# Kernel tuning notes

Measured on AMD Instinct MI355X. Metric: run time of the kernel, lower is better.

## Reference

```python
import jax, jax.numpy as jnp
import numpy as np

GMO_SIGMA = 1.0
EPS_GMO = 1e-16
EPS_BARY = 1e-16
EPS_DIV = 1e-12
CHUNK = 512  # points per search chunk to bound [B, CHUNK, F] intermediates


def _tri_sqdist(p, a, b, c):
    """Exact squared point-to-triangle distance (Ericson).
    p: [B,Pc,1,3], a/b/c: [B,1,F,3] -> [B,Pc,F]"""
    ab = b - a
    ac = c - a
    ap = p - a
    d1 = (ab * ap).sum(-1)
    d2 = (ac * ap).sum(-1)
    bp = p - b
    d3 = (ab * bp).sum(-1)
    d4 = (ac * bp).sum(-1)
    cp_ = p - c
    d5 = (ab * cp_).sum(-1)
    d6 = (ac * cp_).sum(-1)
    va = d3 * d6 - d5 * d4
    vb = d5 * d2 - d1 * d6
    vc = d1 * d4 - d3 * d2
    # candidate closest points per region
    t_ab = d1 / jnp.maximum(d1 - d3, EPS_DIV)
    t_ac = d2 / jnp.maximum(d2 - d6, EPS_DIV)
    t_bc = (d4 - d3) / jnp.maximum((d4 - d3) + (d5 - d6), EPS_DIV)
    den = jnp.maximum(va + vb + vc, EPS_DIV)
    v = (vb / den)[..., None]
    w = (vc / den)[..., None]
    cp = a + v * ab + w * ac  # face interior (default)
    m_bc = (va <= 0) & ((d4 - d3) >= 0) & ((d5 - d6) >= 0)
    m_ac = (vb <= 0) & (d2 >= 0) & (d6 <= 0)
    m_ab = (vc <= 0) & (d1 >= 0) & (d3 <= 0)
    m_a = (d1 <= 0) & (d2 <= 0)
    m_b = (d3 >= 0) & (d4 <= d3)
    m_c = (d6 >= 0) & (d5 <= d6)
    cp = jnp.where(m_bc[..., None], b + t_bc[..., None] * (c - b), cp)
    cp = jnp.where(m_ac[..., None], a + t_ac[..., None] * ac, cp)
    cp = jnp.where(m_ab[..., None], a + t_ab[..., None] * ab, cp)
    cp = jnp.where(m_c[..., None], c, cp)
    cp = jnp.where(m_b[..., None], b, cp)
    cp = jnp.where(m_a[..., None], a, cp)
    return ((p - cp) ** 2).sum(-1)


def _nearest_face_idx(points, tri):
    """points: [B,P,3], tri: [B,F,3,3] -> int32 [B,P] index of nearest face."""
    B, P, _ = points.shape
    a = tri[:, None, :, 0, :]
    b = tri[:, None, :, 1, :]
    c = tri[:, None, :, 2, :]
    nC = P // CHUNK
    pts = points.reshape(B, nC, CHUNK, 3).transpose(1, 0, 2, 3)  # [nC,B,Pc,3]

    def chunk_fn(p):  # p: [B,Pc,3]
        d = _tri_sqdist(p[:, :, None, :], a, b, c)  # [B,Pc,F]
        return jnp.argmin(d, axis=-1)

    idx = jax.lax.map(chunk_fn, pts)  # [nC,B,Pc]
    return idx.transpose(1, 0, 2).reshape(B, P)


def _barycentric(a, b, c, q):
    v1 = b - a
    v2 = c - a
    n = jnp.cross(v1, v2)
    n_dot_n = (n * n).sum(-1)
    n_dot_n = jnp.where(n_dot_n < EPS_BARY, 1.0, n_dot_n)
    w = q - a
    gamma = (jnp.cross(v1, w) * n).sum(-1) / n_dot_n
    beta = (jnp.cross(w, v2) * n).sum(-1) / n_dot_n
    alpha = 1.0 - beta - gamma
    return jnp.stack((alpha, beta, gamma), axis=-1)


def _gmo(sqr_input, sigma):
    sqr_sigma = sigma ** 2
    return jnp.sqrt(sqr_sigma * (sqr_input / (sqr_sigma + sqr_input)) + EPS_GMO)


def setup_inputs() -> dict:
    key = jax.random.key(0)
    k1, k2, k3 = jax.random.split(key, 3)
    points = jax.random.normal(k1, (2, 2048, 3), dtype=jnp.float32)
    mesh_vertices = jax.random.normal(k2, (2, 2562, 3), dtype=jnp.float32)
    mesh_faces = jax.random.randint(k3, (5120, 3), 0, 2562, dtype=jnp.int32)
    return {"points": points, "mesh_vertices": mesh_vertices, "mesh_faces": mesh_faces}


def reference(points, mesh_vertices, mesh_faces):
    B, P, _ = points.shape
    tri = mesh_vertices[:, mesh_faces]  # [B,F,3,3] face vertices
    face_idx = _nearest_face_idx(points, tri)  # [B,P]
    closest_tri = jnp.take_along_axis(tri, face_idx[:, :, None, None], axis=1)  # [B,P,3,3]
    a = closest_tri[:, :, 0, :]
    b = closest_tri[:, :, 1, :]
    c = closest_tri[:, :, 2, :]
    bco = _barycentric(a, b, c, points)  # [B,P,3]
    closest_points = (a * bco[:, :, 0:1] + b * bco[:, :, 1:2] + c * bco[:, :, 2:3])
    square_distances = ((closest_points - points) ** 2).sum(-1)
    robust = _gmo(square_distances, GMO_SIGMA)
    return robust.mean(-1).mean()
```

## Files before the change

### kernel.cpp

```cpp
#include <hip/hip_runtime.h>
#include <math.h>

#define EPS_GMO  1e-16f
#define EPS_BARY 1e-16f
#define EPS_DIV  1e-12f
#define TPB  512
#define RTPB 256
#define GPTS 4
#define FSTRIDE 12
#define QCAP 2048

__global__ void gather_fdat_kernel(const float* __restrict__ verts,
                                   const int* __restrict__ faces,
                                   float* __restrict__ fdat,
                                   int B, int F, int V)
{
    int i = blockIdx.x * blockDim.x + threadIdx.x;
    if (i >= B * F) return;
    int b = i / F;
    int f = i - b * F;
    int i0 = faces[f * 3 + 0], i1 = faces[f * 3 + 1], i2 = faces[f * 3 + 2];
    const float* pa = verts + ((size_t)b * V + i0) * 3;
    const float* pb = verts + ((size_t)b * V + i1) * 3;
    const float* pc = verts + ((size_t)b * V + i2) * 3;
    float ax = pa[0], ay = pa[1], az = pa[2];
    float abx = pb[0] - ax, aby = pb[1] - ay, abz = pb[2] - az;
    float acx = pc[0] - ax, acy = pc[1] - ay, acz = pc[2] - az;
    float saa = abx * abx + aby * aby + abz * abz;
    float sab = abx * acx + aby * acy + abz * acz;
    float scc = acx * acx + acy * acy + acz * acz;
    float* o = fdat + (size_t)i * FSTRIDE;
    o[0] = ax;  o[1] = ay;  o[2] = az;
    o[3] = abx; o[4] = aby; o[5] = abz;
    o[6] = acx; o[7] = acy; o[8] = acz;
    o[9] = saa; o[10] = sab; o[11] = scc;
}

__device__ float tri_sqdist_exact(float px, float py, float pz,
                                  float ax, float ay, float az,
                                  float bx, float by, float bz,
                                  float cx, float cy, float cz)
{
#pragma clang fp contract(off)
    float abx = bx - ax, aby = by - ay, abz = bz - az;
    float acx = cx - ax, acy = cy - ay, acz = cz - az;
    float apx = px - ax, apy = py - ay, apz = pz - az;
    float d1 = abx * apx + aby * apy + abz * apz;
    float d2 = acx * apx + acy * apy + acz * apz;
    float bpx = px - bx, bpy = py - by, bpz = pz - bz;
    float d3 = abx * bpx + aby * bpy + abz * bpz;
    float d4 = acx * bpx + acy * bpy + acz * bpz;
    float cpx_ = px - cx, cpy_ = py - cy, cpz_ = pz - cz;
    float d5 = abx * cpx_ + aby * cpy_ + abz * cpz_;
    float d6 = acx * cpx_ + acy * cpy_ + acz * cpz_;
    float va = d3 * d6 - d5 * d4;
    float vb = d5 * d2 - d1 * d6;
    float vc = d1 * d4 - d3 * d2;
    float t_ab = d1 / fmaxf(d1 - d3, EPS_DIV);
    float t_ac = d2 / fmaxf(d2 - d6, EPS_DIV);
    float t_bc = (d4 - d3) / fmaxf((d4 - d3) + (d5 - d6), EPS_DIV);
    float den = fmaxf(va + vb + vc, EPS_DIV);
    float v = vb / den;
    float w = vc / den;
    float qx = ax + v * abx + w * acx;
    float qy = ay + v * aby + w * acy;
    float qz = az + v * abz + w * acz;
    bool m_bc = (va <= 0.0f) && (d4 - d3 >= 0.0f) && (d5 - d6 >= 0.0f);
    bool m_ac = (vb <= 0.0f) && (d2 >= 0.0f) && (d6 <= 0.0f);
    bool m_ab = (vc <= 0.0f) && (d1 >= 0.0f) && (d3 <= 0.0f);
    bool m_a  = (d1 <= 0.0f) && (d2 <= 0.0f);
    bool m_b  = (d3 >= 0.0f) && (d4 <= d3);
    bool m_c  = (d6 >= 0.0f) && (d5 <= d6);
    if (m_bc) { qx = bx + t_bc * (cx - bx); qy = by + t_bc * (cy - by); qz = bz + t_bc * (cz - bz); }
    if (m_ac) { qx = ax + t_ac * acx;       qy = ay + t_ac * acy;       qz = az + t_ac * acz; }
    if (m_ab) { qx = ax + t_ab * abx;       qy = ay + t_ab * aby;       qz = az + t_ab * abz; }
    if (m_c)  { qx = cx; qy = cy; qz = cz; }
    if (m_b)  { qx = bx; qy = by; qz = bz; }
    if (m_a)  { qx = ax; qy = ay; qz = az; }
    float dx = px - qx, dy = py - qy, dz = pz - qz;
    return dx * dx + dy * dy + dz * dz;
}

__device__ __forceinline__ int dcode(float d)
{
    unsigned raw = __float_as_uint(d) >> 21;
    int c = (int)raw - 380;
    return c < 0 ? 0 : (c > 255 ? 255 : c);
}

__global__ __launch_bounds__(TPB) void p2s_main_kernel(
    const float* __restrict__ points,
    const float* __restrict__ verts,
    const int* __restrict__ faces,
    const float* __restrict__ fdat,
    float* __restrict__ robust_out,
    int P, int V, int F, int npts)
{
    extern __shared__ unsigned dstore32[];
    __shared__ float sd[TPB];
    __shared__ int   si[TPB];
    __shared__ float sT[GPTS];
    __shared__ int   sFace[GPTS];
    __shared__ unsigned squeue[QCAP];
    __shared__ unsigned scnt;

    const int tid = threadIdx.x;
    const int gp0 = blockIdx.x * GPTS;
    const int b   = gp0 / P;

    if (tid == 0) scnt = 0;

    float px[GPTS], py[GPTS], pz[GPTS];
#pragma unroll
    for (int g = 0; g < GPTS; ++g) {
        int gp = gp0 + g; if (gp >= npts) gp = npts - 1;
        const float* pp = points + (size_t)gp * 3;
        px[g] = pp[0]; py[g] = pp[1]; pz[g] = pp[2];
    }

    const float* fb = fdat + (size_t)b * F * FSTRIDE;

    float best[GPTS];
#pragma unroll
    for (int g = 0; g < GPTS; ++g) best[g] = INFINITY;

    for (int f = tid; f < F; f += TPB) {
        const float* fd = fb + (size_t)f * FSTRIDE;
        float4 q0 = *(const float4*)(fd + 0);
        float4 q1 = *(const float4*)(fd + 4);
        float4 q2 = *(const float4*)(fd + 8);
        float ax = q0.x, ay = q0.y, az = q0.z;
        float abx = q0.w, aby = q1.x, abz = q1.y;
        float acx = q1.z, acy = q1.w, acz = q2.x;
        float saa = q2.y, sab = q2.z, scc = q2.w;
        float cbb = saa - 2.0f * sab + scc;
        float det = saa * scc - sab * sab;
        float rsaa = __builtin_amdgcn_rcpf(fmaxf(saa, 1e-30f));
        float rscc = __builtin_amdgcn_rcpf(fmaxf(scc, 1e-30f));
        float rcbb = __builtin_amdgcn_rcpf(fmaxf(cbb, 1e-30f));
        float rdet = __builtin_amdgcn_rcpf(fmaxf(det, 1e-30f));
        float k1 = saa - sab;
        unsigned wcode = 0;
#pragma unroll
        for (int g = 0; g < GPTS; ++g) {
            float apx = px[g] - ax, apy = py[g] - ay, apz = pz[g] - az;
            float sap = apx * apx + apy * apy + apz * apz;
            float d1 = apx * abx + apy * aby + apz * abz;
            float d2 = apx * acx + apy * acy + apz * acz;
            float t0 = __builtin_amdgcn_fmed3f(d1 * rsaa, 0.0f, 1.0f);
            float h0 = d1 + d1;
            float dab = sap - t0 * (h0 - t0 * saa);
            float t1 = __builtin_amdgcn_fmed3f(d2 * rscc, 0.0f, 1.0f);
            float dac = sap - t1 * ((d2 + d2) - t1 * scc);
            float e1 = (d2 - d1) + k1;
            float t2 = __builtin_amdgcn_fmed3f(e1 * rcbb, 0.0f, 1.0f);
            float bpp = (sap - h0) + saa;
            float dbc = bpp - t2 * ((e1 + e1) - t2 * cbb);
            float dmin = fminf(fminf(dab, dac), dbc);
            float vnum = scc * d1 - sab * d2;
            float wnum = saa * d2 - sab * d1;
            bool inside = (vnum >= 0.0f) & (wnum >= 0.0f) & ((vnum + wnum) <= det);
            float idist = sap - (vnum * d1 + wnum * d2) * rdet;
            float d = fmaxf(inside ? fminf(idist, dmin) : dmin, 0.0f);
            wcode |= (unsigned)dcode(d) << (8 * g);
            best[g] = fminf(best[g], d);
        }
        dstore32[f] = wcode;
    }

#pragma unroll
    for (int g = 0; g < GPTS; ++g) {
        sd[tid] = best[g];
        __syncthreads();
        for (int s = TPB / 2; s > 0; s >>= 1) {
            if (tid < s) sd[tid] = fminf(sd[tid], sd[tid + s]);
            __syncthreads();
        }
        if (tid == 0) sT[g] = sd[0] + (1e-4f + 1e-2f * sd[0]);
        __syncthreads();
    }

    int codeT[GPTS];
#pragma unroll
    for (int g = 0; g < GPTS; ++g) codeT[g] = dcode(sT[g]);

    for (int f = tid; f < F; f += TPB) {
        unsigned w = dstore32[f];
#pragma unroll
        for (int g = 0; g < GPTS; ++g) {
            if ((int)((w >> (8 * g)) & 0xffu) <= codeT[g]) {
                unsigned idx = atomicAdd(&scnt, 1u);
                if (idx < QCAP) squeue[idx] = ((unsigned)g << 13) | (unsigned)f;
            }
        }
    }
    __syncthreads();
    unsigned total = scnt;

    float bestE[GPTS]; int bestI[GPTS];
#pragma unroll
    for (int g = 0; g < GPTS; ++g) { bestE[g] = INFINITY; bestI[g] = 0x7fffffff; }

    if (total <= QCAP) {
        for (unsigned q = tid; q < total; q += TPB) {
            unsigned e = squeue[q];
            int g = (int)(e >> 13);
            int f = (int)(e & 0x1fffu);
            int i0 = faces[f * 3 + 0], i1 = faces[f * 3 + 1], i2 = faces[f * 3 + 2];
            const float* pa = verts + ((size_t)b * V + i0) * 3;
            const float* pbv = verts + ((size_t)b * V + i1) * 3;
            const float* pc = verts + ((size_t)b * V + i2) * 3;
            float de = tri_sqdist_exact(px[g], py[g], pz[g],
                                        pa[0], pa[1], pa[2],
                                        pbv[0], pbv[1], pbv[2],
                                        pc[0], pc[1], pc[2]);
            if (de < bestE[g] || (de == bestE[g] && f < bestI[g])) {
                bestE[g] = de; bestI[g] = f;
            }
        }
    } else {
        for (int f = tid; f < F; f += TPB) {
            unsigned w = dstore32[f];
            bool cg[GPTS]; bool any = false;
#pragma unroll
            for (int g = 0; g < GPTS; ++g) {
                cg[g] = (int)((w >> (8 * g)) & 0xffu) <= codeT[g];
                any = any || cg[g];
            }
            if (any) {
                int i0 = faces[f * 3 + 0], i1 = faces[f * 3 + 1], i2 = faces[f * 3 + 2];
                const float* pa = verts + ((size_t)b * V + i0) * 3;
                const float* pbv = verts + ((size_t)b * V + i1) * 3;
                const float* pc = verts + ((size_t)b * V + i2) * 3;
                float ax = pa[0], ay = pa[1], az = pa[2];
                float bx = pbv[0], by = pbv[1], bz = pbv[2];
                float cx = pc[0], cy = pc[1], cz = pc[2];
#pragma unroll
                for (int g = 0; g < GPTS; ++g) {
                    if (cg[g]) {
                        float de = tri_sqdist_exact(px[g], py[g], pz[g],
                                                    ax, ay, az, bx, by, bz, cx, cy, cz);
                        if (de < bestE[g]) { bestE[g] = de; bestI[g] = f; }
                    }
                }
            }
        }
    }

#pragma unroll
    for (int g = 0; g < GPTS; ++g) {
        sd[tid] = bestE[g]; si[tid] = bestI[g];
        __syncthreads();
        for (int s = TPB / 2; s > 0; s >>= 1) {
            if (tid < s) {
                float dv = sd[tid + s]; int iv = si[tid + s];
                if (dv < sd[tid] || (dv == sd[tid] && iv < si[tid])) { sd[tid] = dv; si[tid] = iv; }
            }
            __syncthreads();
        }
        if (tid == 0) sFace[g] = si[0];
        __syncthreads();
    }

    if (tid < GPTS) {
#pragma clang fp contract(off)
        int g = tid;
        int gp = gp0 + g;
        if (gp < npts) {
            int f = sFace[g];
            int i0 = faces[f * 3 + 0], i1 = faces[f * 3 + 1], i2 = faces[f * 3 + 2];
            const float* pa = verts + ((size_t)b * V + i0) * 3;
            const float* pbv = verts + ((size_t)b * V + i1) * 3;
            const float* pc = verts + ((size_t)b * V + i2) * 3;
            float ax = pa[0], ay = pa[1], az = pa[2];
            float bx = pbv[0], by = pbv[1], bz = pbv[2];
            float cx = pc[0], cy = pc[1], cz = pc[2];
            float Px = px[g], Py = py[g], Pz = pz[g];
            float v1x = bx - ax, v1y = by - ay, v1z = bz - az;
            float v2x = cx - ax, v2y = cy - ay, v2z = cz - az;
            float nx = v1y * v2z - v1z * v2y;
            float ny = v1z * v2x - v1x * v2z;
            float nz = v1x * v2y - v1y * v2x;
            float nn = nx * nx + ny * ny + nz * nz;
            if (nn < EPS_BARY) nn = 1.0f;
            float wx = Px - ax, wy = Py - ay, wz = Pz - az;
            float c1x = v1y * wz - v1z * wy;
            float c1y = v1z * wx - v1x * wz;
            float c1z = v1x * wy - v1y * wx;
            float gamma = (c1x * nx + c1y * ny + c1z * nz) / nn;
            float c2x = wy * v2z - wz * v2y;
            float c2y = wz * v2x - wx * v2z;
            float c2z = wx * v2y - wy * v2x;
            float beta = (c2x * nx + c2y * ny + c2z * nz) / nn;
            float alpha = 1.0f - beta - gamma;
            float cpx = ax * alpha + bx * beta + cx * gamma;
            float cpy = ay * alpha + by * beta + cy * gamma;
            float cpz = az * alpha + bz * beta + cz * gamma;
            float dx = cpx - Px, dy = cpy - Py, dz = cpz - Pz;
            float sdist = dx * dx + dy * dy + dz * dz;
            float r = sqrtf(sdist / (1.0f + sdist) + EPS_GMO);
            robust_out[gp] = r;
        }
    }
}

__global__ __launch_bounds__(RTPB) void reduce_mean_kernel(
    const float* __restrict__ vals, float* __restrict__ out, int N, float inv)
{
    __shared__ float s[RTPB];
    int tid = threadIdx.x;
    float acc = 0.0f;
    for (int i = tid; i < N; i += RTPB) acc += vals[i];
    s[tid] = acc;
    __syncthreads();
    for (int st = RTPB / 2; st > 0; st >>= 1) {
        if (tid < st) s[tid] += s[tid + st];
        __syncthreads();
    }
    if (tid == 0) out[0] = s[0] * inv;
}

extern "C" void kernel_launch(void* const* d_in, const int* in_sizes, int n_in,
                              void* d_out, int out_size, void* d_ws, size_t ws_size,
                              hipStream_t stream)
{
    const float* points = (const float*)d_in[0];
    const float* verts  = (const float*)d_in[1];
    const int*   faces  = (const int*)d_in[2];
    float* out = (float*)d_out;

    const int B = 2;
    const int P = in_sizes[0] / (B * 3);
    const int V = in_sizes[1] / (B * 3);
    const int F = in_sizes[2] / 3;
    const int npts = B * P;

    float* fdat   = (float*)d_ws;
    float* robust = fdat + (size_t)B * F * FSTRIDE;

    int nBF = B * F;
    gather_fdat_kernel<<<(nBF + RTPB - 1) / RTPB, RTPB, 0, stream>>>(verts, faces, fdat, B, F, V);

    int nBlocks = (npts + GPTS - 1) / GPTS;
    size_t dynLds = (size_t)F * sizeof(unsigned);
    p2s_main_kernel<<<nBlocks, TPB, dynLds, stream>>>(points, verts, faces, fdat, robust, P, V, F, npts);

    reduce_mean_kernel<<<1, RTPB, 0, stream>>>(robust, out, npts, 1.0f / (float)npts);
}
```

Measured before the change: 57.17 us.

## Keep fast distances in registers and use wave-shuffle reductions

The per-face fast distances now stay in a fully unrolled register array (up to 12 faces × 4 points) instead of quantised 8-bit codes in dynamic LDS, so candidate filtering compares exact floats. The log-step shared-memory min and argmin reductions, each with a barrier per step, are replaced by wave-level xor-shuffle reductions followed by a small cross-wave combine. This removes many __syncthreads and the dynamic LDS allocation, which could allow more blocks per CU. The cost is 48 extra float registers per thread, which may reduce occupancy under 512-thread launch bounds. F is also silently capped at NFK*TPB faces.

New measurement: 58.68 us. +2.6%, slower.

```diff
diff --git a/kernel.cpp b/kernel.cpp
--- a/kernel.cpp
+++ b/kernel.cpp
@@ -6,9 +6,11 @@
 #define EPS_DIV  1e-12f
 #define TPB  512
 #define RTPB 256
+#define NWAVE (TPB / 64)
 #define GPTS 4
 #define FSTRIDE 12
 #define QCAP 2048
+#define NFK 12
 
 __global__ void gather_fdat_kernel(const float* __restrict__ verts,
                                    const int* __restrict__ faces,
@@ -81,13 +83,6 @@
     return dx * dx + dy * dy + dz * dz;
 }
 
-__device__ __forceinline__ int dcode(float d)
-{
-    unsigned raw = __float_as_uint(d) >> 21;
-    int c = (int)raw - 380;
-    return c < 0 ? 0 : (c > 255 ? 255 : c);
-}
-
 __global__ __launch_bounds__(TPB) void p2s_main_kernel(
     const float* __restrict__ points,
     const float* __restrict__ verts,
@@ -96,17 +91,18 @@
     float* __restrict__ robust_out,
     int P, int V, int F, int npts)
 {
-    extern __shared__ unsigned dstore32[];
-    __shared__ float sd[TPB];
-    __shared__ int   si[TPB];
-    __shared__ float sT[GPTS];
+    __shared__ float swmin[NWAVE][GPTS];
+    __shared__ float sargd[NWAVE][GPTS];
+    __shared__ int   sargi[NWAVE][GPTS];
     __shared__ int   sFace[GPTS];
     __shared__ unsigned squeue[QCAP];
     __shared__ unsigned scnt;
 
-    const int tid = threadIdx.x;
-    const int gp0 = blockIdx.x * GPTS;
-    const int b   = gp0 / P;
+    const int tid  = threadIdx.x;
+    const int lane = tid & 63;
+    const int wid  = tid >> 6;
+    const int gp0  = blockIdx.x * GPTS;
+    const int b    = gp0 / P;
 
     if (tid == 0) scnt = 0;
 
@@ -120,11 +116,19 @@
 
     const float* fb = fdat + (size_t)b * F * FSTRIDE;
 
+    float dfast[NFK][GPTS];
     float best[GPTS];
 #pragma unroll
     for (int g = 0; g < GPTS; ++g) best[g] = INFINITY;
-
-    for (int f = tid; f < F; f += TPB) {
+#pragma unroll
+    for (int k = 0; k < NFK; ++k)
+#pragma unroll
+        for (int g = 0; g < GPTS; ++g) dfast[k][g] = INFINITY;
+
+#pragma unroll
+    for (int k = 0; k < NFK; ++k) {
+        int f = tid + k * TPB;
+        if (f >= F) break;
         const float* fd = fb + (size_t)f * FSTRIDE;
         float4 q0 = *(const float4*)(fd + 0);
         float4 q1 = *(const float4*)(fd + 4);
@@ -140,7 +144,6 @@
         float rcbb = __builtin_amdgcn_rcpf(fmaxf(cbb, 1e-30f));
         float rdet = __builtin_amdgcn_rcpf(fmaxf(det, 1e-30f));
         float k1 = saa - sab;
-        unsigned wcode = 0;
 #pragma unroll
         for (int g = 0; g < GPTS; ++g) {
             float apx = px[g] - ax, apy = py[g] - ay, apz = pz[g] - az;
@@ -162,33 +165,39 @@
             bool inside = (vnum >= 0.0f) & (wnum >= 0.0f) & ((vnum + wnum) <= det);
             float idist = sap - (vnum * d1 + wnum * d2) * rdet;
             float d = fmaxf(inside ? fminf(idist, dmin) : dmin, 0.0f);
-            wcode |= (unsigned)dcode(d) << (8 * g);
+            dfast[k][g] = d;
             best[g] = fminf(best[g], d);
         }
-        dstore32[f] = wcode;
-    }
-
+    }
+
+#pragma unroll
+    for (int m = 1; m < 64; m <<= 1) {
+#pragma unroll
+        for (int g = 0; g < GPTS; ++g)
+            best[g] = fminf(best[g], __shfl_xor(best[g], m));
+    }
+    if (lane == 0) {
+#pragma unroll
+        for (int g = 0; g < GPTS; ++g) swmin[wid][g] = best[g];
+    }
+    __syncthreads();
+
+    float Tg[GPTS];
 #pragma unroll
     for (int g = 0; g < GPTS; ++g) {
-        sd[tid] = best[g];
-        __syncthreads();
-        for (int s = TPB / 2; s > 0; s >>= 1) {
-            if (tid < s) sd[tid] = fminf(sd[tid], sd[tid + s]);
-            __syncthreads();
-        }
-        if (tid == 0) sT[g] = sd[0] + (1e-4f + 1e-2f * sd[0]);
-        __syncthreads();
-    }
-
-    int codeT[GPTS];
-#pragma unroll
-    for (int g = 0; g < GPTS; ++g) codeT[g] = dcode(sT[g]);
-
-    for (int f = tid; f < F; f += TPB) {
-        unsigned w = dstore32[f];
+        float mn = swmin[0][g];
+#pragma unroll
+        for (int w = 1; w < NWAVE; ++w) mn = fminf(mn, swmin[w][g]);
+        Tg[g] = mn + (1e-4f + 1e-2f * mn);
+    }
+
+#pragma unroll
+    for (int k = 0; k < NFK; ++k) {
+        int f = tid + k * TPB;
+        if (f >= F) break;
 #pragma unroll
         for (int g = 0; g < GPTS; ++g) {
-            if ((int)((w >> (8 * g)) & 0xffu) <= codeT[g]) {
+            if (dfast[k][g] <= Tg[g]) {
                 unsigned idx = atomicAdd(&scnt, 1u);
                 if (idx < QCAP) squeue[idx] = ((unsigned)g << 13) | (unsigned)f;
             }
@@ -219,14 +228,13 @@
             }
         }
     } else {
-        for (int f = tid; f < F; f += TPB) {
-            unsigned w = dstore32[f];
-            bool cg[GPTS]; bool any = false;
-#pragma unroll
-            for (int g = 0; g < GPTS; ++g) {
-                cg[g] = (int)((w >> (8 * g)) & 0xffu) <= codeT[g];
-                any = any || cg[g];
-            }
+#pragma unroll
+        for (int k = 0; k < NFK; ++k) {
+            int f = tid + k * TPB;
+            if (f >= F) break;
+            bool any = false;
+#pragma unroll
+            for (int g = 0; g < GPTS; ++g) any = any || (dfast[k][g] <= Tg[g]);
             if (any) {
                 int i0 = faces[f * 3 + 0], i1 = faces[f * 3 + 1], i2 = faces[f * 3 + 2];
                 const float* pa = verts + ((size_t)b * V + i0) * 3;
@@ -237,7 +245,7 @@
                 float cx = pc[0], cy = pc[1], cz = pc[2];
 #pragma unroll
                 for (int g = 0; g < GPTS; ++g) {
-                    if (cg[g]) {
+                    if (dfast[k][g] <= Tg[g]) {
                         float de = tri_sqdist_exact(px[g], py[g], pz[g],
                                                     ax, ay, az, bx, by, bz, cx, cy, cz);
                         if (de < bestE[g]) { bestE[g] = de; bestI[g] = f; }
@@ -248,19 +256,35 @@
     }
 
 #pragma unroll
-    for (int g = 0; g < GPTS; ++g) {
-        sd[tid] = bestE[g]; si[tid] = bestI[g];
-        __syncthreads();
-        for (int s = TPB / 2; s > 0; s >>= 1) {
-            if (tid < s) {
-                float dv = sd[tid + s]; int iv = si[tid + s];
-                if (dv < sd[tid] || (dv == sd[tid] && iv < si[tid])) { sd[tid] = dv; si[tid] = iv; }
-            }
-            __syncthreads();
-        }
-        if (tid == 0) sFace[g] = si[0];
-        __syncthreads();
-    }
+    for (int m = 1; m < 64; m <<= 1) {
+#pragma unroll
+        for (int g = 0; g < GPTS; ++g) {
+            float od = __shfl_xor(bestE[g], m);
+            int   oi = __shfl_xor(bestI[g], m);
+            if (od < bestE[g] || (od == bestE[g] && oi < bestI[g])) {
+                bestE[g] = od; bestI[g] = oi;
+            }
+        }
+    }
+    if (lane == 0) {
+#pragma unroll
+        for (int g = 0; g < GPTS; ++g) { sargd[wid][g] = bestE[g]; sargi[wid][g] = bestI[g]; }
+    }
+    __syncthreads();
+
+    if (tid == 0) {
+#pragma unroll
+        for (int g = 0; g < GPTS; ++g) {
+            float dmn = sargd[0][g]; int imn = sargi[0][g];
+#pragma unroll
+            for (int w = 1; w < NWAVE; ++w) {
+                float dv = sargd[w][g]; int iv = sargi[w][g];
+                if (dv < dmn || (dv == dmn && iv < imn)) { dmn = dv; imn = iv; }
+            }
+            sFace[g] = imn;
+        }
+    }
+    __syncthreads();
 
     if (tid < GPTS) {
 #pragma clang fp contract(off)
@@ -342,8 +366,7 @@
     gather_fdat_kernel<<<(nBF + RTPB - 1) / RTPB, RTPB, 0, stream>>>(verts, faces, fdat, B, F, V);
 
     int nBlocks = (npts + GPTS - 1) / GPTS;
-    size_t dynLds = (size_t)F * sizeof(unsigned);
-    p2s_main_kernel<<<nBlocks, TPB, dynLds, stream>>>(points, verts, faces, fdat, robust, P, V, F, npts);
+    p2s_main_kernel<<<nBlocks, TPB, 0, stream>>>(points, verts, faces, fdat, robust, P, V, F, npts);
 
     reduce_mean_kernel<<<1, RTPB, 0, stream>>>(robust, out, npts, 1.0f / (float)npts);
 }
```
